# Optimization experiments

Hardware: AMD Instinct MI355X
Metric: run time of the kernel (lower is better)

## Reference

```python
import jax, jax.numpy as jnp
import numpy as np

B, T, F, UNITS = 64, 512, 128, 512
EPS = 1e-3  # Keras LayerNormalization default epsilon


def _layer_norm(x, g, b):
    m = x.mean(-1, keepdims=True)
    v = x.var(-1, keepdims=True)
    return (x - m) * jax.lax.rsqrt(v + EPS) * g + b


def _lstm(x, W, U, b):
    # Keras LSTM, gate order [i, f, c, o], zero initial state, tanh activations.
    Bsz = x.shape[0]
    Un = U.shape[0]
    h0 = jnp.zeros((Bsz, Un), x.dtype)
    c0 = jnp.zeros((Bsz, Un), x.dtype)
    xW = x @ W + b  # precompute input projection: [B, T, 4U]

    def step(carry, xw_t):
        h, c = carry
        z = xw_t + h @ U
        i, f, g, o = jnp.split(z, 4, axis=-1)
        c = jax.nn.sigmoid(f) * c + jax.nn.sigmoid(i) * jnp.tanh(g)
        h = jax.nn.sigmoid(o) * jnp.tanh(c)
        return (h, c), h

    (h, c), hs = jax.lax.scan(step, (h0, c0), jnp.swapaxes(xW, 0, 1))
    return jnp.swapaxes(hs, 0, 1), h, c  # seq out [B,T,U], final h, c


def _block(x, l0, l1, Wt, bt):
    block_in = x
    # layer 0: LSTM -> LayerNorm
    W, U, b, g, be = l0
    h, _, _ = _lstm(x, W, U, b)
    out = _layer_norm(h, g, be)
    # layer 1: LSTM -> LayerNorm -> Highway (units match layer 0)
    W, U, b, g, be = l1
    h, _, _ = _lstm(out, W, U, b)
    Hx = _layer_norm(h, g, be)
    Tx = jax.nn.sigmoid(out @ Wt + bt)  # transform gate, bias init -1.5
    hw = Hx * Tx + (1.0 - Tx) * out
    # quasi-dense: concat block input with last layer output
    return jnp.concatenate([block_in, hw], axis=-1)


def setup_inputs() -> dict:
    key = jax.random.key(0)
    ks = iter(jax.random.split(key, 32))
    def nrm(shape, scale):
        return jax.random.normal(next(ks), shape, jnp.float32) * scale
    d = {"x": jax.random.normal(next(ks), (B, T, F), jnp.float32)}
    in_dims = {"00": F, "01": UNITS, "10": F + UNITS, "11": UNITS}
    for tag, ind in in_dims.items():
        d[f"W{tag}"] = nrm((ind, 4 * UNITS), 1.0 / np.sqrt(ind))
        d[f"U{tag}"] = nrm((UNITS, 4 * UNITS), 1.0 / np.sqrt(UNITS))
        d[f"b{tag}"] = jnp.zeros((4 * UNITS,), jnp.float32)
        d[f"g{tag}"] = jnp.ones((UNITS,), jnp.float32)
        d[f"be{tag}"] = jnp.zeros((UNITS,), jnp.float32)
    for blk in ("0", "1"):
        d[f"Wt{blk}"] = nrm((UNITS, UNITS), 1.0 / np.sqrt(UNITS))
        d[f"bt{blk}"] = jnp.full((UNITS,), -1.5, jnp.float32)
    return d


def reference(x,
              W00, U00, b00, g00, be00,
              W01, U01, b01, g01, be01,
              Wt0, bt0,
              W10, U10, b10, g10, be10,
              W11, U11, b11, g11, be11,
              Wt1, bt1):
    out0 = _block(x, (W00, U00, b00, g00, be00), (W01, U01, b01, g01, be01), Wt0, bt0)
    out1 = _block(out0, (W10, U10, b10, g10, be10), (W11, U11, b11, g11, be11), Wt1, bt1)
    return out1  # [B, T, F + 2*UNITS]
```

## Files before the change

kernel.cpp:

```cpp
#include <hip/hip_runtime.h>
#include <hip/hip_bf16.h>

typedef unsigned short u16;
typedef unsigned int u32;
typedef __attribute__((ext_vector_type(8))) short short8;
typedef __attribute__((ext_vector_type(4))) short short4v;
typedef __attribute__((ext_vector_type(4))) float float4v;
typedef __attribute__((ext_vector_type(2))) unsigned int uint2v;
typedef __attribute__((ext_vector_type(4))) unsigned int uint4v;

#define Bsz 64
#define Tsz 512
#define Fsz 128
#define Usz 512
#define Gsz 2048
#define Msz 32768
#define OUTW 1152
#define BINW 640
#define NWG 16
#define FLSTR 32

__device__ __forceinline__ u16 f2b(float f) {
  u32 u = __float_as_uint(f);
  u32 r = (u + 0x7fffu + ((u >> 16) & 1u)) >> 16;
  return (u16)r;
}
__device__ __forceinline__ float b2f(u16 h) {
  return __uint_as_float(((u32)h) << 16);
}
__device__ __forceinline__ float sigm(float x) { return 1.f / (1.f + __expf(-x)); }
__device__ __forceinline__ float tanhfast(float x) { return 2.f / (1.f + __expf(-2.f * x)) - 1.f; }

__global__ void k_wt(const float* __restrict__ src, u16* __restrict__ dst, int K, int N) {
  __shared__ float t[32][33];
  int k0 = blockIdx.y << 5, n0 = blockIdx.x << 5;
  int tid = threadIdx.x;
  int r = tid >> 3, c = (tid & 7) << 2;
  float4v v = *(const float4v*)(src + (size_t)(k0 + r) * N + n0 + c);
  t[r][c + 0] = v[0]; t[r][c + 1] = v[1]; t[r][c + 2] = v[2]; t[r][c + 3] = v[3];
  __syncthreads();
  short4v o;
  o[0] = (short)f2b(t[c + 0][r]);
  o[1] = (short)f2b(t[c + 1][r]);
  o[2] = (short)f2b(t[c + 2][r]);
  o[3] = (short)f2b(t[c + 3][r]);
  *(short4v*)(dst + (size_t)(n0 + r) * K + k0 + c) = o;
}

__global__ void k_cvx(const float* __restrict__ x, float* __restrict__ dout, u16* __restrict__ bin) {
  int id = blockIdx.x * 256 + threadIdx.x;
  int row = id >> 5, c = (id & 31) << 2;
  float4v v = *(const float4v*)(x + (size_t)row * Fsz + c);
  *(float4v*)(dout + (size_t)row * OUTW + c) = v;
  short4v o;
  o[0] = (short)f2b(v[0]); o[1] = (short)f2b(v[1]);
  o[2] = (short)f2b(v[2]); o[3] = (short)f2b(v[3]);
  *(short4v*)(bin + (size_t)row * BINW + c) = o;
}

template <int APERM, int CPERM>
__launch_bounds__(256)
__global__ void k_gemm(const u16* __restrict__ A, int lda,
                       const u16* __restrict__ Bt, int K, int N,
                       const float* __restrict__ bias,
                       u16* __restrict__ C) {
  __shared__ u16 Al[128][40];
  __shared__ u16 Bl[64][40];
  int tid = threadIdx.x;
  int lane = tid & 63, wid = tid >> 6;
  int n0 = blockIdx.x << 6;
  size_t m0 = (size_t)blockIdx.y << 7;
  int mr = lane & 15, ko = (lane >> 4) << 3;
  float4v acc[2][4];
#pragma unroll
  for (int i = 0; i < 2; ++i)
#pragma unroll
    for (int j = 0; j < 4; ++j) acc[i][j] = (float4v){0.f, 0.f, 0.f, 0.f};

  for (int k0 = 0; k0 < K; k0 += 32) {
#pragma unroll
    for (int i = 0; i < 2; ++i) {
      int id = tid + (i << 8);
      int row = id >> 2, kc = (id & 3) << 3;
      int mlog = (int)m0 + row;
      size_t rp = APERM ? ((size_t)(mlog & 63) << 9) + (mlog >> 6) : (size_t)mlog;
      *(short8*)&Al[row][kc] = *(const short8*)(A + rp * (size_t)lda + k0 + kc);
    }
    {
      int row = tid >> 2, kc = (tid & 3) << 3;
      *(short8*)&Bl[row][kc] = *(const short8*)(Bt + (size_t)(n0 + row) * K + k0 + kc);
    }
    __syncthreads();
    short8 af0 = *(short8*)&Al[(wid << 5) + mr][ko];
    short8 af1 = *(short8*)&Al[(wid << 5) + 16 + mr][ko];
    short8 bf0 = *(short8*)&Bl[mr][ko];
    short8 bf1 = *(short8*)&Bl[16 + mr][ko];
    short8 bf2 = *(short8*)&Bl[32 + mr][ko];
    short8 bf3 = *(short8*)&Bl[48 + mr][ko];
    acc[0][0] = __builtin_amdgcn_mfma_f32_16x16x32_bf16(af0, bf0, acc[0][0], 0, 0, 0);
    acc[0][1] = __builtin_amdgcn_mfma_f32_16x16x32_bf16(af0, bf1, acc[0][1], 0, 0, 0);
    acc[0][2] = __builtin_amdgcn_mfma_f32_16x16x32_bf16(af0, bf2, acc[0][2], 0, 0, 0);
    acc[0][3] = __builtin_amdgcn_mfma_f32_16x16x32_bf16(af0, bf3, acc[0][3], 0, 0, 0);
    acc[1][0] = __builtin_amdgcn_mfma_f32_16x16x32_bf16(af1, bf0, acc[1][0], 0, 0, 0);
    acc[1][1] = __builtin_amdgcn_mfma_f32_16x16x32_bf16(af1, bf1, acc[1][1], 0, 0, 0);
    acc[1][2] = __builtin_amdgcn_mfma_f32_16x16x32_bf16(af1, bf2, acc[1][2], 0, 0, 0);
    acc[1][3] = __builtin_amdgcn_mfma_f32_16x16x32_bf16(af1, bf3, acc[1][3], 0, 0, 0);
    __syncthreads();
  }
  int rbase = (lane >> 4) << 2;
#pragma unroll
  for (int mt = 0; mt < 2; ++mt)
#pragma unroll
    for (int nt = 0; nt < 4; ++nt) {
      int n = n0 + (nt << 4) + mr;
      float bv = bias[n];
#pragma unroll
      for (int r = 0; r < 4; ++r) {
        int mlog = (int)m0 + (wid << 5) + (mt << 4) + rbase + r;
        float val = acc[mt][nt][r] + bv;
        if (CPERM) {
          int b = mlog & 63, tt = mlog >> 6;
          int u = n & 511, g = n >> 9;
          C[((((size_t)tt * 512 + u) * 64 + b) << 2) + g] = f2b(val);
        } else {
          C[(size_t)mlog * N + n] = f2b(val);
        }
      }
    }
}

__global__ void k_zero(u32* __restrict__ p, int n32) {
  int id = blockIdx.x * 256 + threadIdx.x;
  for (int i = id; i < n32; i += gridDim.x * 256) p[i] = 0u;
}

__launch_bounds__(256, 1)
__global__ void k_scan(const u16* __restrict__ xw2,
                       const u16* __restrict__ Ut,
                       u16* __restrict__ hn,
                       u16* __restrict__ hseq,
                       u32* __restrict__ bar) {
  __shared__ u16 hl[32768];
  __shared__ u16 hout[2048];
  int wg = blockIdx.x;
  int tid = threadIdx.x;
  int lane = tid & 63, wid = tid >> 6;
  int mr = lane & 15, cg = lane >> 4;
  int gate = mr & 3, du = mr >> 2;
  int u0 = (wg << 5) + (wid << 3);

  short8 af[2][16];
#pragma unroll
  for (int mt = 0; mt < 2; ++mt) {
    size_t urow = (size_t)(gate * Usz + u0 + (mt << 2) + du) * Usz;
#pragma unroll
    for (int kk = 0; kk < 16; ++kk)
      af[mt][kk] = *(const short8*)(Ut + urow + (kk << 5) + (cg << 3));
  }

  float cst[2][4];
#pragma unroll
  for (int mt = 0; mt < 2; ++mt)
#pragma unroll
    for (int nt = 0; nt < 4; ++nt) cst[mt][nt] = 0.f;

  short4v xwc[2][4], xwn[2][4];
#pragma unroll
  for (int mt = 0; mt < 2; ++mt)
#pragma unroll
    for (int nt = 0; nt < 4; ++nt)
      xwc[mt][nt] = *(const short4v*)(xw2 + ((((size_t)0 * 512 + u0 + (mt << 2) + cg) * 64
                                             + (nt << 4) + mr) << 2));

  for (int t = 0; t < Tsz; ++t) {
    const u16* rbuf = hn + ((t & 1) ? 32768 : 0);
    u16* wbuf = hn + ((t & 1) ? 0 : 32768);

    float4v acc[2][4];
#pragma unroll
    for (int mt = 0; mt < 2; ++mt)
#pragma unroll
      for (int nt = 0; nt < 4; ++nt)
        acc[mt][nt] = (float4v){b2f((u16)xwc[mt][nt][0]), b2f((u16)xwc[mt][nt][1]),
                                b2f((u16)xwc[mt][nt][2]), b2f((u16)xwc[mt][nt][3])};

    if (t + 1 < Tsz) {
#pragma unroll
      for (int mt = 0; mt < 2; ++mt)
#pragma unroll
        for (int nt = 0; nt < 4; ++nt)
          xwn[mt][nt] = *(const short4v*)(xw2 + ((((size_t)(t + 1) * 512 + u0 + (mt << 2) + cg) * 64
                                                 + (nt << 4) + mr) << 2));
    }

    if (t > 0) {
      if (wid == 0) {
        u32 tgt = (u32)t;
        for (;;) {
          u32 v = (lane < NWG)
                    ? __hip_atomic_load(bar + lane * FLSTR, __ATOMIC_RELAXED, __HIP_MEMORY_SCOPE_AGENT)
                    : 0xFFFFFFFFu;
          if (__all(v >= tgt)) break;
          __builtin_amdgcn_s_sleep(1);
        }
        __threadfence();
      }
      __syncthreads();

      {
        const char* hsrc = (const char*)rbuf;
#pragma unroll
        for (int j = 0; j < 16; ++j) {
          int c = (wid << 4) + j;
          const char* src = hsrc + ((((c & 3) << 4) + mr) << 10) + ((c >> 2) << 6) + (cg << 4);
          __builtin_amdgcn_global_load_lds(
              (const __attribute__((address_space(1))) void*)src,
              (__attribute__((address_space(3))) void*)(hl + (c << 9)),
              16, 0, 0);
        }
      }
      __syncthreads();

#pragma unroll
      for (int kk = 0; kk < 16; ++kk) {
        short8 bfr[4];
#pragma unroll
        for (int nt = 0; nt < 4; ++nt)
          bfr[nt] = *(const short8*)(hl + ((((kk << 2) + nt) << 9) + (lane << 3)));
#pragma unroll
        for (int mt = 0; mt < 2; ++mt)
#pragma unroll
          for (int nt = 0; nt < 4; ++nt)
            acc[mt][nt] = __builtin_amdgcn_mfma_f32_16x16x32_bf16(af[mt][kk], bfr[nt], acc[mt][nt], 0, 0, 0);
      }
    }

    u16 hb[2][4];
#pragma unroll
    for (int mt = 0; mt < 2; ++mt)
#pragma unroll
      for (int nt = 0; nt < 4; ++nt) {
        float zi = acc[mt][nt][0], zf = acc[mt][nt][1];
        float zg = acc[mt][nt][2], zo = acc[mt][nt][3];
        float c = sigm(zf) * cst[mt][nt] + sigm(zi) * tanhfast(zg);
        cst[mt][nt] = c;
        hb[mt][nt] = f2b(sigm(zo) * tanhfast(c));
      }

#pragma unroll
    for (int mt = 0; mt < 2; ++mt)
#pragma unroll
      for (int nt = 0; nt < 4; ++nt) {
        int b = (nt << 4) + mr;
        int ul = (wid << 3) + (mt << 2) + cg;
        *(u16*)((char*)hout + (b << 6) + ((ul << 1) ^ ((b & 7) << 3))) = hb[mt][nt];
      }
    __syncthreads();

    {
      int b = tid >> 2, q = tid & 3, s = (b & 7) << 3;
      const char* hrow = (const char*)hout + (b << 6);
      uint2v A0 = *(const uint2v*)(hrow + (((q << 4) | 0) ^ s));
      uint2v A1 = *(const uint2v*)(hrow + (((q << 4) | 8) ^ s));
      uint4v val; val[0] = A0[0]; val[1] = A0[1]; val[2] = A1[0]; val[3] = A1[1];
      *(uint4v*)((char*)wbuf + (b << 10) + (wg << 6) + (q << 4)) = val;
      *(uint4v*)((char*)hseq + ((size_t)t << 16) + (b << 10) + (wg << 6) + (q << 4)) = val;
    }
    __syncthreads();

    if (tid == 0)
      __hip_atomic_store(bar + wg * FLSTR, (u32)(t + 1), __ATOMIC_RELEASE, __HIP_MEMORY_SCOPE_AGENT);

    if (t + 1 < Tsz) {
#pragma unroll
      for (int mt = 0; mt < 2; ++mt)
#pragma unroll
        for (int nt = 0; nt < 4; ++nt) xwc[mt][nt] = xwn[mt][nt];
    }
  }
}

__launch_bounds__(256)
__global__ void k_ln(const u16* __restrict__ in, const float* __restrict__ g,
                     const float* __restrict__ be, u16* __restrict__ out) {
  int lane = threadIdx.x & 63, wid = threadIdx.x >> 6;
  size_t row = (size_t)blockIdx.x * 4 + wid;
  short8 v = *(const short8*)(in + row * Usz + (lane << 3));
  float f[8];
  float s = 0.f, q = 0.f;
#pragma unroll
  for (int j = 0; j < 8; ++j) { f[j] = b2f((u16)v[j]); s += f[j]; q += f[j] * f[j]; }
#pragma unroll
  for (int o = 32; o > 0; o >>= 1) { s += __shfl_xor(s, o); q += __shfl_xor(q, o); }
  float mean = s * (1.f / 512.f);
  float var = q * (1.f / 512.f) - mean * mean;
  float rs = rsqrtf(var + 1e-3f);
  float4v g0 = *(const float4v*)(g + (lane << 3));
  float4v g1 = *(const float4v*)(g + (lane << 3) + 4);
  float4v e0 = *(const float4v*)(be + (lane << 3));
  float4v e1 = *(const float4v*)(be + (lane << 3) + 4);
  short8 o8;
#pragma unroll
  for (int j = 0; j < 8; ++j) {
    float gg = (j < 4) ? g0[j] : g1[j - 4];
    float ee = (j < 4) ? e0[j] : e1[j - 4];
    o8[j] = (short)f2b((f[j] - mean) * rs * gg + ee);
  }
  *(short8*)(out + row * Usz + (lane << 3)) = o8;
}

__launch_bounds__(256)
__global__ void k_lnhw(const u16* __restrict__ hs, const float* __restrict__ g,
                       const float* __restrict__ be, const u16* __restrict__ txr,
                       const u16* __restrict__ ob, float* __restrict__ dout,
                       int dcol, u16* __restrict__ bin) {
  int lane = threadIdx.x & 63, wid = threadIdx.x >> 6;
  size_t row = (size_t)blockIdx.x * 4 + wid;
  short8 v = *(const short8*)(hs + row * Usz + (lane << 3));
  float f[8];
  float s = 0.f, q = 0.f;
#pragma unroll
  for (int j = 0; j < 8; ++j) { f[j] = b2f((u16)v[j]); s += f[j]; q += f[j] * f[j]; }
#pragma unroll
  for (int o = 32; o > 0; o >>= 1) { s += __shfl_xor(s, o); q += __shfl_xor(q, o); }
  float mean = s * (1.f / 512.f);
  float var = q * (1.f / 512.f) - mean * mean;
  float rs = rsqrtf(var + 1e-3f);
  float4v g0 = *(const float4v*)(g + (lane << 3));
  float4v g1 = *(const float4v*)(g + (lane << 3) + 4);
  float4v e0 = *(const float4v*)(be + (lane << 3));
  float4v e1 = *(const float4v*)(be + (lane << 3) + 4);
  short8 tv = *(const short8*)(txr + row * Usz + (lane << 3));
  short8 ov = *(const short8*)(ob + row * Usz + (lane << 3));
  float hwv[8];
#pragma unroll
  for (int j = 0; j < 8; ++j) {
    float gg = (j < 4) ? g0[j] : g1[j - 4];
    float ee = (j < 4) ? e0[j] : e1[j - 4];
    float hx = (f[j] - mean) * rs * gg + ee;
    float tx = sigm(b2f((u16)tv[j]));
    float o_ = b2f((u16)ov[j]);
    hwv[j] = hx * tx + (1.f - tx) * o_;
  }
  size_t orow = ((row & 63) << 9) + (row >> 6);
  float4v w0 = {hwv[0], hwv[1], hwv[2], hwv[3]};
  float4v w1 = {hwv[4], hwv[5], hwv[6], hwv[7]};
  *(float4v*)(dout + orow * OUTW + dcol + (lane << 3)) = w0;
  *(float4v*)(dout + orow * OUTW + dcol + (lane << 3) + 4) = w1;
  if (bin) {
    short8 hb;
#pragma unroll
    for (int j = 0; j < 8; ++j) hb[j] = (short)f2b(hwv[j]);
    *(short8*)(bin + orow * BINW + 128 + (lane << 3)) = hb;
  }
}

extern "C" void kernel_launch(void* const* d_in, const int* in_sizes, int n_in,
                              void* d_out, int out_size, void* d_ws, size_t ws_size,
                              hipStream_t stream) {
  (void)in_sizes; (void)n_in; (void)out_size; (void)ws_size;
  const float* x = (const float*)d_in[0];
  const float* W[4]  = {(const float*)d_in[1],  (const float*)d_in[6],
                        (const float*)d_in[11], (const float*)d_in[16]};
  const float* U[4]  = {(const float*)d_in[2],  (const float*)d_in[7],
                        (const float*)d_in[12], (const float*)d_in[17]};
  const float* bb_[4] = {(const float*)d_in[3],  (const float*)d_in[8],
                        (const float*)d_in[13], (const float*)d_in[18]};
  const float* gg_[4] = {(const float*)d_in[4],  (const float*)d_in[9],
                        (const float*)d_in[14], (const float*)d_in[19]};
  const float* be_[4] = {(const float*)d_in[5],  (const float*)d_in[10],
                        (const float*)d_in[15], (const float*)d_in[20]};
  const float* Wtr[2] = {(const float*)d_in[21], (const float*)d_in[23]};
  const float* btr[2] = {(const float*)d_in[22], (const float*)d_in[24]};

  char* ws = (char*)d_ws;
  size_t off = 0;
  u16* xwb  = (u16*)(ws + off); off += (size_t)Msz * Gsz * 2;
  u16* hseq = (u16*)(ws + off); off += (size_t)Msz * Usz * 2;
  u16* mid  = (u16*)(ws + off); off += (size_t)Msz * Usz * 2;
  u16* bin  = (u16*)(ws + off); off += (size_t)Msz * BINW * 2;
  const int KIN[4] = {128, 512, 640, 512};
  u16* Wtb[4];
  for (int i = 0; i < 4; ++i) { Wtb[i] = (u16*)(ws + off); off += (size_t)Gsz * KIN[i] * 2; }
  u16* Utb[4];
  for (int i = 0; i < 4; ++i) { Utb[i] = (u16*)(ws + off); off += (size_t)Gsz * Usz * 2; }
  u16* Wtrb[2];
  for (int i = 0; i < 2; ++i) { Wtrb[i] = (u16*)(ws + off); off += (size_t)Usz * Usz * 2; }
  u16* hn = (u16*)(ws + off); off += 2 * (size_t)Bsz * Usz * 2;
  u32* bar = (u32*)(ws + off); off += 4096;
  float* dout = (float*)d_out;

  for (int i = 0; i < 4; ++i)
    k_wt<<<dim3(Gsz / 32, KIN[i] / 32), 256, 0, stream>>>(W[i], Wtb[i], KIN[i], Gsz);
  for (int i = 0; i < 4; ++i)
    k_wt<<<dim3(Gsz / 32, Usz / 32), 256, 0, stream>>>(U[i], Utb[i], Usz, Gsz);
  for (int i = 0; i < 2; ++i)
    k_wt<<<dim3(Usz / 32, Usz / 32), 256, 0, stream>>>(Wtr[i], Wtrb[i], Usz, Usz);

  k_cvx<<<(Msz * 32) / 256, 256, 0, stream>>>(x, dout, bin);

  for (int blk = 0; blk < 2; ++blk) {
    int l0 = blk * 2, l1 = blk * 2 + 1;
    k_gemm<1, 1><<<dim3(Gsz / 64, Msz / 128), 256, 0, stream>>>(bin, BINW, Wtb[l0], KIN[l0], Gsz, bb_[l0], xwb);
    k_zero<<<1, 256, 0, stream>>>(bar, NWG * FLSTR);
    k_scan<<<NWG, 256, 0, stream>>>(xwb, Utb[l0], hn, hseq, bar);
    k_ln<<<Msz / 4, 256, 0, stream>>>(hseq, gg_[l0], be_[l0], mid);
    k_gemm<0, 1><<<dim3(Gsz / 64, Msz / 128), 256, 0, stream>>>(mid, Usz, Wtb[l1], Usz, Gsz, bb_[l1], xwb);
    k_zero<<<1, 256, 0, stream>>>(bar, NWG * FLSTR);
    k_scan<<<NWG, 256, 0, stream>>>(xwb, Utb[l1], hn, hseq, bar);
    k_gemm<0, 0><<<dim3(Usz / 64, Msz / 128), 256, 0, stream>>>(mid, Usz, Wtrb[blk], Usz, Usz, btr[blk], xwb);
    k_lnhw<<<Msz / 4, 256, 0, stream>>>(hseq, gg_[l1], be_[l1], xwb, mid, dout,
                                        blk == 0 ? 128 : 640, blk == 0 ? bin : (u16*)nullptr);
  }
}
```

Measured before the change: 14.04 ms.

## Wavefront-pipeline both LSTM layers in one persistent scan kernel with folded LayerNorm

Merges the layer-0 and layer-1 recurrences into one 32-workgroup persistent kernel. Sixteen workgroups run layer 0 and sixteen run layer 1 one timestep behind, coordinated through per-workgroup flags and a 4-deep ring of h0 buffers. Layer 1 computes its input projection on the fly from raw h0: the LayerNorm gamma is folded into W, and the beta and mean terms are precomputed as per-gate vectors p and q. Layer 1 also writes the normalized mid tensor for the highway step. This removes the separate LayerNorm pass and the layer-1 input GEMM, and overlaps the two serial scans. In exchange, each layer-1 step does twice the MFMA work, and the extra cross-workgroup flag polling adds latency to the critical path.

```diff
diff --git a/kernel.cpp b/kernel.cpp
--- a/kernel.cpp
+++ b/kernel.cpp
@@ -3,9 +3,11 @@
 
 typedef unsigned short u16;
 typedef unsigned int u32;
+typedef unsigned long long u64;
 typedef __attribute__((ext_vector_type(8))) short short8;
 typedef __attribute__((ext_vector_type(4))) short short4v;
 typedef __attribute__((ext_vector_type(4))) float float4v;
+typedef __attribute__((ext_vector_type(2))) float float2v;
 typedef __attribute__((ext_vector_type(2))) unsigned int uint2v;
 typedef __attribute__((ext_vector_type(4))) unsigned int uint4v;
 
@@ -31,13 +33,16 @@
 __device__ __forceinline__ float sigm(float x) { return 1.f / (1.f + __expf(-x)); }
 __device__ __forceinline__ float tanhfast(float x) { return 2.f / (1.f + __expf(-2.f * x)) - 1.f; }
 
-__global__ void k_wt(const float* __restrict__ src, u16* __restrict__ dst, int K, int N) {
+__global__ void k_wt(const float* __restrict__ src, u16* __restrict__ dst, int K, int N,
+                     const float* __restrict__ scale) {
   __shared__ float t[32][33];
   int k0 = blockIdx.y << 5, n0 = blockIdx.x << 5;
   int tid = threadIdx.x;
   int r = tid >> 3, c = (tid & 7) << 2;
   float4v v = *(const float4v*)(src + (size_t)(k0 + r) * N + n0 + c);
-  t[r][c + 0] = v[0]; t[r][c + 1] = v[1]; t[r][c + 2] = v[2]; t[r][c + 3] = v[3];
+  float s = scale ? scale[k0 + r] : 1.f;
+  t[r][c + 0] = v[0] * s; t[r][c + 1] = v[1] * s;
+  t[r][c + 2] = v[2] * s; t[r][c + 3] = v[3] * s;
   __syncthreads();
   short4v o;
   o[0] = (short)f2b(t[c + 0][r]);
@@ -45,6 +50,18 @@
   o[2] = (short)f2b(t[c + 2][r]);
   o[3] = (short)f2b(t[c + 3][r]);
   *(short4v*)(dst + (size_t)(n0 + r) * K + k0 + c) = o;
+}
+
+__global__ void k_pq(const float* __restrict__ W, const float* __restrict__ g,
+                     const float* __restrict__ be, const float* __restrict__ b1,
+                     float* __restrict__ p, float* __restrict__ q) {
+  int n = blockIdx.x * 256 + threadIdx.x;
+  float sp = 0.f, sq = 0.f;
+  for (int k = 0; k < Usz; ++k) {
+    float w = W[(size_t)k * Gsz + n];
+    sp += w * g[k]; sq += w * be[k];
+  }
+  p[n] = sp; q[n] = sq + b1[n];
 }
 
 __global__ void k_cvx(const float* __restrict__ x, float* __restrict__ dout, u16* __restrict__ bin) {
@@ -135,72 +152,203 @@
 }
 
 __launch_bounds__(256, 1)
-__global__ void k_scan(const u16* __restrict__ xw2,
-                       const u16* __restrict__ Ut,
-                       u16* __restrict__ hn,
-                       u16* __restrict__ hseq,
-                       u32* __restrict__ bar) {
-  __shared__ u16 hl[32768];
+__global__ void k_scan2(const u16* __restrict__ xw2,
+                        const u16* __restrict__ Ut0,
+                        const u16* __restrict__ Wg1,
+                        const u16* __restrict__ Ut1,
+                        const float* __restrict__ p1,
+                        const float* __restrict__ q1,
+                        const float* __restrict__ g0v,
+                        const float* __restrict__ be0v,
+                        u16* __restrict__ hn0,
+                        u16* __restrict__ hn1,
+                        u16* __restrict__ h1seq,
+                        u16* __restrict__ mid,
+                        u32* __restrict__ bar) {
+  __shared__ u16 hl0[32768];
+  __shared__ u16 hl1[32768];
   __shared__ u16 hout[2048];
-  int wg = blockIdx.x;
+  __shared__ float stats[128];
   int tid = threadIdx.x;
   int lane = tid & 63, wid = tid >> 6;
   int mr = lane & 15, cg = lane >> 4;
   int gate = mr & 3, du = mr >> 2;
-  int u0 = (wg << 5) + (wid << 3);
-
-  short8 af[2][16];
-#pragma unroll
-  for (int mt = 0; mt < 2; ++mt) {
-    size_t urow = (size_t)(gate * Usz + u0 + (mt << 2) + du) * Usz;
-#pragma unroll
-    for (int kk = 0; kk < 16; ++kk)
-      af[mt][kk] = *(const short8*)(Ut + urow + (kk << 5) + (cg << 3));
-  }
-
-  float cst[2][4];
-#pragma unroll
-  for (int mt = 0; mt < 2; ++mt)
-#pragma unroll
-    for (int nt = 0; nt < 4; ++nt) cst[mt][nt] = 0.f;
-
-  short4v xwc[2][4], xwn[2][4];
-#pragma unroll
-  for (int mt = 0; mt < 2; ++mt)
-#pragma unroll
-    for (int nt = 0; nt < 4; ++nt)
-      xwc[mt][nt] = *(const short4v*)(xw2 + ((((size_t)0 * 512 + u0 + (mt << 2) + cg) * 64
-                                             + (nt << 4) + mr) << 2));
-
-  for (int t = 0; t < Tsz; ++t) {
-    const u16* rbuf = hn + ((t & 1) ? 32768 : 0);
-    u16* wbuf = hn + ((t & 1) ? 0 : 32768);
-
-    float4v acc[2][4];
+
+  if (blockIdx.x < 16) {
+    int w = blockIdx.x;
+    int u0 = (w << 5) + (wid << 3);
+    short8 af[2][16];
+#pragma unroll
+    for (int mt = 0; mt < 2; ++mt) {
+      size_t urow = (size_t)(gate * Usz + u0 + (mt << 2) + du) * Usz;
+#pragma unroll
+      for (int kk = 0; kk < 16; ++kk)
+        af[mt][kk] = *(const short8*)(Ut0 + urow + (kk << 5) + (cg << 3));
+    }
+    float cst[2][4];
 #pragma unroll
     for (int mt = 0; mt < 2; ++mt)
 #pragma unroll
+      for (int nt = 0; nt < 4; ++nt) cst[mt][nt] = 0.f;
+
+    short4v xwc[2][4], xwn[2][4];
+#pragma unroll
+    for (int mt = 0; mt < 2; ++mt)
+#pragma unroll
       for (int nt = 0; nt < 4; ++nt)
-        acc[mt][nt] = (float4v){b2f((u16)xwc[mt][nt][0]), b2f((u16)xwc[mt][nt][1]),
-                                b2f((u16)xwc[mt][nt][2]), b2f((u16)xwc[mt][nt][3])};
-
-    if (t + 1 < Tsz) {
+        xwc[mt][nt] = *(const short4v*)(xw2 + ((((size_t)0 * 512 + u0 + (mt << 2) + cg) * 64
+                                               + (nt << 4) + mr) << 2));
+
+    for (int t = 0; t < Tsz; ++t) {
+      float4v acc[2][4];
 #pragma unroll
       for (int mt = 0; mt < 2; ++mt)
 #pragma unroll
         for (int nt = 0; nt < 4; ++nt)
-          xwn[mt][nt] = *(const short4v*)(xw2 + ((((size_t)(t + 1) * 512 + u0 + (mt << 2) + cg) * 64
-                                                 + (nt << 4) + mr) << 2));
-    }
-
-    if (t > 0) {
+          acc[mt][nt] = (float4v){b2f((u16)xwc[mt][nt][0]), b2f((u16)xwc[mt][nt][1]),
+                                  b2f((u16)xwc[mt][nt][2]), b2f((u16)xwc[mt][nt][3])};
+      if (t + 1 < Tsz) {
+#pragma unroll
+        for (int mt = 0; mt < 2; ++mt)
+#pragma unroll
+          for (int nt = 0; nt < 4; ++nt)
+            xwn[mt][nt] = *(const short4v*)(xw2 + ((((size_t)(t + 1) * 512 + u0 + (mt << 2) + cg) * 64
+                                                   + (nt << 4) + mr) << 2));
+      }
+
+      if (t > 0) {
+        if (wid == 0) {
+          for (;;) {
+            int pass = 1;
+            if (lane < 16) {
+              u32 v = __hip_atomic_load(bar + lane * FLSTR, __ATOMIC_RELAXED, __HIP_MEMORY_SCOPE_AGENT);
+              pass = (v >= (u32)t);
+            } else if (lane < 32 && t >= 4) {
+              u32 v = __hip_atomic_load(bar + 2048 + (lane - 16) * FLSTR, __ATOMIC_RELAXED, __HIP_MEMORY_SCOPE_AGENT);
+              pass = (v >= (u32)(t - 3));
+            }
+            if (__all(pass)) break;
+            __builtin_amdgcn_s_sleep(1);
+          }
+          __threadfence();
+        }
+        __syncthreads();
+
+        {
+          const char* hsrc = (const char*)(hn0 + (size_t)((t - 1) & 3) * 32768);
+#pragma unroll
+          for (int j = 0; j < 16; ++j) {
+            int c = (wid << 4) + j;
+            const char* src = hsrc + ((((c & 3) << 4) + mr) << 10) + ((c >> 2) << 6) + (cg << 4);
+            __builtin_amdgcn_global_load_lds(
+                (const __attribute__((address_space(1))) void*)src,
+                (__attribute__((address_space(3))) void*)(hl0 + (c << 9)),
+                16, 0, 0);
+          }
+        }
+        __syncthreads();
+
+#pragma unroll
+        for (int kk = 0; kk < 16; ++kk) {
+          short8 bfr[4];
+#pragma unroll
+          for (int nt = 0; nt < 4; ++nt)
+            bfr[nt] = *(const short8*)(hl0 + ((((kk << 2) + nt) << 9) + (lane << 3)));
+#pragma unroll
+          for (int mt = 0; mt < 2; ++mt)
+#pragma unroll
+            for (int nt = 0; nt < 4; ++nt)
+              acc[mt][nt] = __builtin_amdgcn_mfma_f32_16x16x32_bf16(af[mt][kk], bfr[nt], acc[mt][nt], 0, 0, 0);
+        }
+      }
+
+      u16 hb[2][4];
+#pragma unroll
+      for (int mt = 0; mt < 2; ++mt)
+#pragma unroll
+        for (int nt = 0; nt < 4; ++nt) {
+          float zi = acc[mt][nt][0], zf = acc[mt][nt][1];
+          float zg = acc[mt][nt][2], zo = acc[mt][nt][3];
+          float c = sigm(zf) * cst[mt][nt] + sigm(zi) * tanhfast(zg);
+          cst[mt][nt] = c;
+          hb[mt][nt] = f2b(sigm(zo) * tanhfast(c));
+        }
+
+#pragma unroll
+      for (int mt = 0; mt < 2; ++mt)
+#pragma unroll
+        for (int nt = 0; nt < 4; ++nt) {
+          int b = (nt << 4) + mr;
+          int ul = (wid << 3) + (mt << 2) + cg;
+          *(u16*)((char*)hout + (b << 6) + ((ul << 1) ^ ((b & 7) << 3))) = hb[mt][nt];
+        }
+      __syncthreads();
+
+      {
+        int b = tid >> 2, q = tid & 3, s = (b & 7) << 3;
+        const char* hrow = (const char*)hout + (b << 6);
+        uint2v A0 = *(const uint2v*)(hrow + (((q << 4) | 0) ^ s));
+        uint2v A1 = *(const uint2v*)(hrow + (((q << 4) | 8) ^ s));
+        uint4v val; val[0] = A0[0]; val[1] = A0[1]; val[2] = A1[0]; val[3] = A1[1];
+        *(uint4v*)((char*)(hn0 + (size_t)(t & 3) * 32768) + (b << 10) + (w << 6) + (q << 4)) = val;
+      }
+      __syncthreads();
+
+      if (tid == 0)
+        __hip_atomic_store(bar + w * FLSTR, (u32)(t + 1), __ATOMIC_RELEASE, __HIP_MEMORY_SCOPE_AGENT);
+
+      if (t + 1 < Tsz) {
+#pragma unroll
+        for (int mt = 0; mt < 2; ++mt)
+#pragma unroll
+          for (int nt = 0; nt < 4; ++nt) xwc[mt][nt] = xwn[mt][nt];
+      }
+    }
+  } else {
+    int w = blockIdx.x - 16;
+    int u0 = (w << 5) + (wid << 3);
+    short8 afw[2][16], afu[2][16];
+#pragma unroll
+    for (int mt = 0; mt < 2; ++mt) {
+      size_t urow = (size_t)(gate * Usz + u0 + (mt << 2) + du) * Usz;
+#pragma unroll
+      for (int kk = 0; kk < 16; ++kk) {
+        afw[mt][kk] = *(const short8*)(Wg1 + urow + (kk << 5) + (cg << 3));
+        afu[mt][kk] = *(const short8*)(Ut1 + urow + (kk << 5) + (cg << 3));
+      }
+    }
+    float pv[2][4], qv[2][4];
+#pragma unroll
+    for (int mt = 0; mt < 2; ++mt)
+#pragma unroll
+      for (int r = 0; r < 4; ++r) {
+        int n = r * 512 + u0 + (mt << 2) + cg;
+        pv[mt][r] = p1[n]; qv[mt][r] = q1[n];
+      }
+    float gv[8], bev[8];
+#pragma unroll
+    for (int j = 0; j < 8; ++j) {
+      gv[j] = g0v[(w << 5) + (cg << 3) + j];
+      bev[j] = be0v[(w << 5) + (cg << 3) + j];
+    }
+    float cst[2][4];
+#pragma unroll
+    for (int mt = 0; mt < 2; ++mt)
+#pragma unroll
+      for (int nt = 0; nt < 4; ++nt) cst[mt][nt] = 0.f;
+
+    for (int t = 0; t < Tsz; ++t) {
       if (wid == 0) {
-        u32 tgt = (u32)t;
         for (;;) {
-          u32 v = (lane < NWG)
-                    ? __hip_atomic_load(bar + lane * FLSTR, __ATOMIC_RELAXED, __HIP_MEMORY_SCOPE_AGENT)
-                    : 0xFFFFFFFFu;
-          if (__all(v >= tgt)) break;
+          int pass = 1;
+          if (lane < 16) {
+            u32 v = __hip_atomic_load(bar + lane * FLSTR, __ATOMIC_RELAXED, __HIP_MEMORY_SCOPE_AGENT);
+            pass = (v >= (u32)(t + 1));
+          } else if (lane < 32 && t > 0) {
+            u32 v = __hip_atomic_load(bar + 2048 + (lane - 16) * FLSTR, __ATOMIC_RELAXED, __HIP_MEMORY_SCOPE_AGENT);
+            pass = (v >= (u32)t);
+          }
+          if (__all(pass)) break;
           __builtin_amdgcn_s_sleep(1);
         }
         __threadfence();
@@ -208,105 +356,141 @@
       __syncthreads();
 
       {
-        const char* hsrc = (const char*)rbuf;
+        const char* hsrc = (const char*)(hn0 + (size_t)(t & 3) * 32768);
 #pragma unroll
         for (int j = 0; j < 16; ++j) {
           int c = (wid << 4) + j;
           const char* src = hsrc + ((((c & 3) << 4) + mr) << 10) + ((c >> 2) << 6) + (cg << 4);
           __builtin_amdgcn_global_load_lds(
               (const __attribute__((address_space(1))) void*)src,
-              (__attribute__((address_space(3))) void*)(hl + (c << 9)),
+              (__attribute__((address_space(3))) void*)(hl0 + (c << 9)),
               16, 0, 0);
         }
       }
+      if (t > 0) {
+        const char* hsrc = (const char*)(hn1 + (size_t)((t - 1) & 1) * 32768);
+#pragma unroll
+        for (int j = 0; j < 16; ++j) {
+          int c = (wid << 4) + j;
+          const char* src = hsrc + ((((c & 3) << 4) + mr) << 10) + ((c >> 2) << 6) + (cg << 4);
+          __builtin_amdgcn_global_load_lds(
+              (const __attribute__((address_space(1))) void*)src,
+              (__attribute__((address_space(3))) void*)(hl1 + (c << 9)),
+              16, 0, 0);
+        }
+      }
       __syncthreads();
 
+      {
+        float s = 0.f, sq = 0.f;
+#pragma unroll
+        for (int kk = 0; kk < 16; ++kk) {
+          short8 hv = *(const short8*)(hl0 + ((((kk << 2) + wid) << 9) + (lane << 3)));
+#pragma unroll
+          for (int j = 0; j < 8; ++j) { float x = b2f((u16)hv[j]); s += x; sq += x * x; }
+        }
+        s += __shfl_xor(s, 16); s += __shfl_xor(s, 32);
+        sq += __shfl_xor(sq, 16); sq += __shfl_xor(sq, 32);
+        float m = s * (1.f / 512.f);
+        float var = sq * (1.f / 512.f) - m * m;
+        float rs = rsqrtf(var + 1e-3f);
+        if (lane < 16) { stats[((wid << 4) + lane) * 2] = m; stats[((wid << 4) + lane) * 2 + 1] = rs; }
+      }
+
+      float4v aW[2][4], aU[2][4];
+#pragma unroll
+      for (int mt = 0; mt < 2; ++mt)
+#pragma unroll
+        for (int nt = 0; nt < 4; ++nt) { aW[mt][nt] = (float4v){0.f,0.f,0.f,0.f}; aU[mt][nt] = (float4v){0.f,0.f,0.f,0.f}; }
 #pragma unroll
       for (int kk = 0; kk < 16; ++kk) {
         short8 bfr[4];
 #pragma unroll
         for (int nt = 0; nt < 4; ++nt)
-          bfr[nt] = *(const short8*)(hl + ((((kk << 2) + nt) << 9) + (lane << 3)));
+          bfr[nt] = *(const short8*)(hl0 + ((((kk << 2) + nt) << 9) + (lane << 3)));
 #pragma unroll
         for (int mt = 0; mt < 2; ++mt)
 #pragma unroll
           for (int nt = 0; nt < 4; ++nt)
-            acc[mt][nt] = __builtin_amdgcn_mfma_f32_16x16x32_bf16(af[mt][kk], bfr[nt], acc[mt][nt], 0, 0, 0);
-      }
-    }
-
-    u16 hb[2][4];
-#pragma unroll
-    for (int mt = 0; mt < 2; ++mt)
+            aW[mt][nt] = __builtin_amdgcn_mfma_f32_16x16x32_bf16(afw[mt][kk], bfr[nt], aW[mt][nt], 0, 0, 0);
+      }
+      if (t > 0) {
+#pragma unroll
+        for (int kk = 0; kk < 16; ++kk) {
+          short8 bfr[4];
+#pragma unroll
+          for (int nt = 0; nt < 4; ++nt)
+            bfr[nt] = *(const short8*)(hl1 + ((((kk << 2) + nt) << 9) + (lane << 3)));
+#pragma unroll
+          for (int mt = 0; mt < 2; ++mt)
+#pragma unroll
+            for (int nt = 0; nt < 4; ++nt)
+              aU[mt][nt] = __builtin_amdgcn_mfma_f32_16x16x32_bf16(afu[mt][kk], bfr[nt], aU[mt][nt], 0, 0, 0);
+        }
+      }
+      __syncthreads();
+
+      float2v mrs[4];
+#pragma unroll
+      for (int nt = 0; nt < 4; ++nt)
+        mrs[nt] = *(const float2v*)&stats[((nt << 4) + mr) * 2];
+
+      u16 hb[2][4];
+#pragma unroll
+      for (int mt = 0; mt < 2; ++mt)
+#pragma unroll
+        for (int nt = 0; nt < 4; ++nt) {
+          float m = mrs[nt][0], rs = mrs[nt][1];
+          float z0 = rs * (aW[mt][nt][0] - m * pv[mt][0]) + qv[mt][0] + aU[mt][nt][0];
+          float z1 = rs * (aW[mt][nt][1] - m * pv[mt][1]) + qv[mt][1] + aU[mt][nt][1];
+          float z2 = rs * (aW[mt][nt][2] - m * pv[mt][2]) + qv[mt][2] + aU[mt][nt][2];
+          float z3 = rs * (aW[mt][nt][3] - m * pv[mt][3]) + qv[mt][3] + aU[mt][nt][3];
+          float c = sigm(z1) * cst[mt][nt] + sigm(z0) * tanhfast(z2);
+          cst[mt][nt] = c;
+          hb[mt][nt] = f2b(sigm(z3) * tanhfast(c));
+        }
+
+#pragma unroll
+      for (int mt = 0; mt < 2; ++mt)
+#pragma unroll
+        for (int nt = 0; nt < 4; ++nt) {
+          int b = (nt << 4) + mr;
+          int ul = (wid << 3) + (mt << 2) + cg;
+          *(u16*)((char*)hout + (b << 6) + ((ul << 1) ^ ((b & 7) << 3))) = hb[mt][nt];
+        }
+      __syncthreads();
+
+      uint4v val;
+      {
+        int b = tid >> 2, q = tid & 3, s = (b & 7) << 3;
+        const char* hrow = (const char*)hout + (b << 6);
+        uint2v A0 = *(const uint2v*)(hrow + (((q << 4) | 0) ^ s));
+        uint2v A1 = *(const uint2v*)(hrow + (((q << 4) | 8) ^ s));
+        val[0] = A0[0]; val[1] = A0[1]; val[2] = A1[0]; val[3] = A1[1];
+        *(uint4v*)((char*)(hn1 + (size_t)(t & 1) * 32768) + (b << 10) + (w << 6) + (q << 4)) = val;
+      }
+      __syncthreads();
+
+      if (tid == 0)
+        __hip_atomic_store(bar + 2048 + w * FLSTR, (u32)(t + 1), __ATOMIC_RELEASE, __HIP_MEMORY_SCOPE_AGENT);
+
+      {
+        int b = tid >> 2, q = tid & 3;
+        *(uint4v*)((char*)h1seq + ((size_t)t << 16) + (b << 10) + (w << 6) + (q << 4)) = val;
+      }
 #pragma unroll
       for (int nt = 0; nt < 4; ++nt) {
-        float zi = acc[mt][nt][0], zf = acc[mt][nt][1];
-        float zg = acc[mt][nt][2], zo = acc[mt][nt][3];
-        float c = sigm(zf) * cst[mt][nt] + sigm(zi) * tanhfast(zg);
-        cst[mt][nt] = c;
-        hb[mt][nt] = f2b(sigm(zo) * tanhfast(c));
-      }
-
-#pragma unroll
-    for (int mt = 0; mt < 2; ++mt)
-#pragma unroll
-      for (int nt = 0; nt < 4; ++nt) {
+        short8 hv = *(const short8*)(hl0 + ((((w << 2) + nt) << 9) + (lane << 3)));
+        float m = mrs[nt][0], rs = mrs[nt][1];
+        short8 o8;
+#pragma unroll
+        for (int j = 0; j < 8; ++j)
+          o8[j] = (short)f2b((b2f((u16)hv[j]) - m) * rs * gv[j] + bev[j]);
         int b = (nt << 4) + mr;
-        int ul = (wid << 3) + (mt << 2) + cg;
-        *(u16*)((char*)hout + (b << 6) + ((ul << 1) ^ ((b & 7) << 3))) = hb[mt][nt];
-      }
-    __syncthreads();
-
-    {
-      int b = tid >> 2, q = tid & 3, s = (b & 7) << 3;
-      const char* hrow = (const char*)hout + (b << 6);
-      uint2v A0 = *(const uint2v*)(hrow + (((q << 4) | 0) ^ s));
-      uint2v A1 = *(const uint2v*)(hrow + (((q << 4) | 8) ^ s));
-      uint4v val; val[0] = A0[0]; val[1] = A0[1]; val[2] = A1[0]; val[3] = A1[1];
-      *(uint4v*)((char*)wbuf + (b << 10) + (wg << 6) + (q << 4)) = val;
-      *(uint4v*)((char*)hseq + ((size_t)t << 16) + (b << 10) + (wg << 6) + (q << 4)) = val;
-    }
-    __syncthreads();
-
-    if (tid == 0)
-      __hip_atomic_store(bar + wg * FLSTR, (u32)(t + 1), __ATOMIC_RELEASE, __HIP_MEMORY_SCOPE_AGENT);
-
-    if (t + 1 < Tsz) {
-#pragma unroll
-      for (int mt = 0; mt < 2; ++mt)
-#pragma unroll
-        for (int nt = 0; nt < 4; ++nt) xwc[mt][nt] = xwn[mt][nt];
+        *(short8*)(mid + ((size_t)t * 64 + b) * Usz + (w << 5) + (cg << 3)) = o8;
+      }
     }
   }
-}
-
-__launch_bounds__(256)
-__global__ void k_ln(const u16* __restrict__ in, const float* __restrict__ g,
-                     const float* __restrict__ be, u16* __restrict__ out) {
-  int lane = threadIdx.x & 63, wid = threadIdx.x >> 6;
-  size_t row = (size_t)blockIdx.x * 4 + wid;
-  short8 v = *(const short8*)(in + row * Usz + (lane << 3));
-  float f[8];
-  float s = 0.f, q = 0.f;
-#pragma unroll
-  for (int j = 0; j < 8; ++j) { f[j] = b2f((u16)v[j]); s += f[j]; q += f[j] * f[j]; }
-#pragma unroll
-  for (int o = 32; o > 0; o >>= 1) { s += __shfl_xor(s, o); q += __shfl_xor(q, o); }
-  float mean = s * (1.f / 512.f);
-  float var = q * (1.f / 512.f) - mean * mean;
-  float rs = rsqrtf(var + 1e-3f);
-  float4v g0 = *(const float4v*)(g + (lane << 3));
-  float4v g1 = *(const float4v*)(g + (lane << 3) + 4);
-  float4v e0 = *(const float4v*)(be + (lane << 3));
-  float4v e1 = *(const float4v*)(be + (lane << 3) + 4);
-  short8 o8;
-#pragma unroll
-  for (int j = 0; j < 8; ++j) {
-    float gg = (j < 4) ? g0[j] : g1[j - 4];
-    float ee = (j < 4) ? e0[j] : e1[j - 4];
-    o8[j] = (short)f2b((f[j] - mean) * rs * gg + ee);
-  }
-  *(short8*)(out + row * Usz + (lane << 3)) = o8;
 }
 
 __launch_bounds__(256)
@@ -375,10 +559,10 @@
 
   char* ws = (char*)d_ws;
   size_t off = 0;
-  u16* xwb  = (u16*)(ws + off); off += (size_t)Msz * Gsz * 2;
-  u16* hseq = (u16*)(ws + off); off += (size_t)Msz * Usz * 2;
-  u16* mid  = (u16*)(ws + off); off += (size_t)Msz * Usz * 2;
-  u16* bin  = (u16*)(ws + off); off += (size_t)Msz * BINW * 2;
+  u16* xwb   = (u16*)(ws + off); off += (size_t)Msz * Gsz * 2;
+  u16* h1seq = (u16*)(ws + off); off += (size_t)Msz * Usz * 2;
+  u16* mid   = (u16*)(ws + off); off += (size_t)Msz * Usz * 2;
+  u16* bin   = (u16*)(ws + off); off += (size_t)Msz * BINW * 2;
   const int KIN[4] = {128, 512, 640, 512};
   u16* Wtb[4];
   for (int i = 0; i < 4; ++i) { Wtb[i] = (u16*)(ws + off); off += (size_t)Gsz * KIN[i] * 2; }
@@ -386,30 +570,34 @@
   for (int i = 0; i < 4; ++i) { Utb[i] = (u16*)(ws + off); off += (size_t)Gsz * Usz * 2; }
   u16* Wtrb[2];
   for (int i = 0; i < 2; ++i) { Wtrb[i] = (u16*)(ws + off); off += (size_t)Usz * Usz * 2; }
-  u16* hn = (u16*)(ws + off); off += 2 * (size_t)Bsz * Usz * 2;
-  u32* bar = (u32*)(ws + off); off += 4096;
+  float* pq = (float*)(ws + off); off += 4 * Gsz * 4;
+  u16* hn0 = (u16*)(ws + off); off += 4 * (size_t)Bsz * Usz * 2;
+  u16* hn1 = (u16*)(ws + off); off += 2 * (size_t)Bsz * Usz * 2;
+  u32* bar = (u32*)(ws + off); off += 16384;
   float* dout = (float*)d_out;
 
+  k_wt<<<dim3(Gsz / 32, KIN[0] / 32), 256, 0, stream>>>(W[0], Wtb[0], KIN[0], Gsz, nullptr);
+  k_wt<<<dim3(Gsz / 32, KIN[1] / 32), 256, 0, stream>>>(W[1], Wtb[1], KIN[1], Gsz, gg_[0]);
+  k_wt<<<dim3(Gsz / 32, KIN[2] / 32), 256, 0, stream>>>(W[2], Wtb[2], KIN[2], Gsz, nullptr);
+  k_wt<<<dim3(Gsz / 32, KIN[3] / 32), 256, 0, stream>>>(W[3], Wtb[3], KIN[3], Gsz, gg_[2]);
   for (int i = 0; i < 4; ++i)
-    k_wt<<<dim3(Gsz / 32, KIN[i] / 32), 256, 0, stream>>>(W[i], Wtb[i], KIN[i], Gsz);
-  for (int i = 0; i < 4; ++i)
-    k_wt<<<dim3(Gsz / 32, Usz / 32), 256, 0, stream>>>(U[i], Utb[i], Usz, Gsz);
+    k_wt<<<dim3(Gsz / 32, Usz / 32), 256, 0, stream>>>(U[i], Utb[i], Usz, Gsz, nullptr);
   for (int i = 0; i < 2; ++i)
-    k_wt<<<dim3(Usz / 32, Usz / 32), 256, 0, stream>>>(Wtr[i], Wtrb[i], Usz, Usz);
+    k_wt<<<dim3(Usz / 32, Usz / 32), 256, 0, stream>>>(Wtr[i], Wtrb[i], Usz, Usz, nullptr);
+  k_pq<<<8, 256, 0, stream>>>(W[1], gg_[0], be_[0], bb_[1], pq + 0 * Gsz, pq + 1 * Gsz);
+  k_pq<<<8, 256, 0, stream>>>(W[3], gg_[2], be_[2], bb_[3], pq + 2 * Gsz, pq + 3 * Gsz);
 
   k_cvx<<<(Msz * 32) / 256, 256, 0, stream>>>(x, dout, bin);
 
   for (int blk = 0; blk < 2; ++blk) {
     int l0 = blk * 2, l1 = blk * 2 + 1;
     k_gemm<1, 1><<<dim3(Gsz / 64, Msz / 128), 256, 0, stream>>>(bin, BINW, Wtb[l0], KIN[l0], Gsz, bb_[l0], xwb);
-    k_zero<<<1, 256, 0, stream>>>(bar, NWG * FLSTR);
-    k_scan<<<NWG, 256, 0, stream>>>(xwb, Utb[l0], hn, hseq, bar);
-    k_ln<<<Msz / 4, 256, 0, stream>>>(hseq, gg_[l0], be_[l0], mid);
-    k_gemm<0, 1><<<dim3(Gsz / 64, Msz / 128), 256, 0, stream>>>(mid, Usz, Wtb[l1], Usz, Gsz, bb_[l1], xwb);
-    k_zero<<<1, 256, 0, stream>>>(bar, NWG * FLSTR);
-    k_scan<<<NWG, 256, 0, stream>>>(xwb, Utb[l1], hn, hseq, bar);
+    k_zero<<<1, 256, 0, stream>>>(bar, 4096);
+    k_scan2<<<32, 256, 0, stream>>>(xwb, Utb[l0], Wtb[l1], Utb[l1],
+                                    pq + (blk * 2 + 0) * Gsz, pq + (blk * 2 + 1) * Gsz,
+                                    gg_[l0], be_[l0], hn0, hn1, h1seq, mid, bar);
     k_gemm<0, 0><<<dim3(Usz / 64, Msz / 128), 256, 0, stream>>>(mid, Usz, Wtrb[blk], Usz, Usz, btr[blk], xwb);
-    k_lnhw<<<Msz / 4, 256, 0, stream>>>(hseq, gg_[l1], be_[l1], xwb, mid, dout,
+    k_lnhw<<<Msz / 4, 256, 0, stream>>>(h1seq, gg_[l1], be_[l1], xwb, mid, dout,
                                         blk == 0 ? 128 : 640, blk == 0 ? bin : (u16*)nullptr);
   }
 }
```

Result: faster. 12.02 ms (-14.4%).
